# Performance work log

Hardware: AMD Instinct MI355X
Metric: run time of the kernel (lower is better)

## Reference

```python
import jax, jax.numpy as jnp
import numpy as np

B, A, S, D, OUT = 8, 16384, 2048, 512, 512
REDUCTION = "mean"  # matches init_kwargs


def setup_inputs() -> dict:
    key = jax.random.key(0)
    k1, k2, k3 = jax.random.split(key, 3)
    input_rep = jax.random.normal(k1, (B, A, D), jnp.float32)
    # sorted residue ids per protein (atoms are stored residue-by-residue)
    aa_res_ids = jnp.sort(jax.random.randint(k2, (B, A), 0, S), axis=-1).astype(jnp.int32)
    input_aa_len = jnp.full((B,), A, jnp.int32)
    input_seq_len = jnp.full((B,), S, jnp.int32)
    W = jax.random.normal(k3, (OUT, D), jnp.float32) / np.sqrt(D)
    bias = jnp.zeros((OUT,), jnp.float32)
    return {"input_rep": input_rep, "aa_res_ids": aa_res_ids,
            "input_aa_len": input_aa_len, "input_seq_len": input_seq_len,
            "W": W, "bias": bias}


def _pool(input_rep, aa_res_ids, input_aa_len, input_seq_len):
    # input_rep: [B, A, D]; aa_res_ids: [B, A] in [0, S)
    Bv, Av, Dv = input_rep.shape
    valid = jnp.arange(Av)[None, :] < input_aa_len[:, None]          # [B, A] atoms within aa_len
    seg = jnp.arange(Bv)[:, None] * S + aa_res_ids                   # flatten (b, res_id) -> segment id
    seg = jnp.where(valid, seg, Bv * S)                              # invalid atoms -> dummy segment
    nseg = Bv * S + 1
    seg_f = seg.reshape(-1)
    counts = jax.ops.segment_sum(valid.reshape(-1).astype(input_rep.dtype), seg_f,
                                 num_segments=nseg)[: Bv * S].reshape(Bv, S)
    if REDUCTION == "mean":
        sums = jax.ops.segment_sum(input_rep.reshape(Bv * Av, Dv), seg_f,
                                   num_segments=nseg)[: Bv * S].reshape(Bv, S, Dv)
        pooled = sums / jnp.maximum(counts, 1)[..., None]
    elif REDUCTION == "max":
        vals = jnp.where(valid[..., None], input_rep, -jnp.inf).reshape(Bv * Av, Dv)
        pooled = jax.ops.segment_max(vals, seg_f, num_segments=nseg)[: Bv * S].reshape(Bv, S, Dv)
        pooled = jnp.where((counts > 0)[..., None], pooled, 0.0)
    else:
        raise ValueError("Unsupported reduction method: {}".format(REDUCTION))
    in_seq = jnp.arange(S)[None, :] < input_seq_len[:, None]         # [B, S] positions within seq_len
    filled = (counts > 0) & in_seq                                   # residues that received >=1 atom
    n_fill = filled.sum(axis=1)                                      # [B]
    avg = (pooled * filled[..., None]).sum(axis=1) / jnp.maximum(n_fill, 1)[:, None].astype(input_rep.dtype)
    # unfilled-but-in-range positions get the per-protein average of filled residues; out-of-range stay 0
    out = jnp.where(filled[..., None], pooled,
                    jnp.where(in_seq[..., None], avg[:, None, :], jnp.zeros((), input_rep.dtype)))
    return out


def reference(input_rep, aa_res_ids, input_aa_len, input_seq_len, W, bias):
    out = _pool(input_rep, aa_res_ids, input_aa_len, input_seq_len)  # [B, S, D]
    return out @ W.T + bias                                          # [B, S, OUT]
```

## Files before the change

### kernel.cpp

```cpp
#include <hip/hip_runtime.h>
#include <cstdint>
#include <cstddef>

#define Bv 8
#define Av 16384
#define Sv 2048
#define Dv 512
#define OUTv 512
#define Mv (Bv * Sv)

using u16 = unsigned short;
using f32x4 = __attribute__((ext_vector_type(4))) float;
using bf16x8 = __attribute__((ext_vector_type(8))) short;

__device__ __forceinline__ u16 f2bf(float x) {
  union { float f; uint32_t u; } v; v.f = x;
  uint32_t u = v.u;
  uint32_t r = u + 0x7FFFu + ((u >> 16) & 1u);
  return (u16)(r >> 16);
}
__device__ __forceinline__ float bf2f(u16 h) {
  union { uint32_t u; float f; } v; v.u = ((uint32_t)h) << 16; return v.f;
}

__global__ __launch_bounds__(128)
void pool_kernel(const float* __restrict__ rep, const int* __restrict__ res_ids,
                 const int* __restrict__ aa_len, u16* __restrict__ pooled,
                 int* __restrict__ counts) {
  const int bs = blockIdx.x;
  const int b = bs >> 11;
  const int s = bs & (Sv - 1);
  int alen = aa_len[b];
  alen = alen < 0 ? 0 : (alen > Av ? Av : alen);
  const int* ids = res_ids + b * Av;
  int lo = 0, hi = alen;
  while (lo < hi) { int mid = (lo + hi) >> 1; if (ids[mid] < s) lo = mid + 1; else hi = mid; }
  const int start = lo;
  hi = alen;
  while (lo < hi) { int mid = (lo + hi) >> 1; if (ids[mid] <= s) lo = mid + 1; else hi = mid; }
  const int end = lo;
  const int cnt = end - start;

  const int t = threadIdx.x;
  float a0 = 0.f, a1 = 0.f, a2 = 0.f, a3 = 0.f;
  const float* base = rep + (size_t)b * Av * Dv + t * 4;
  for (int a = start; a < end; ++a) {
    float4 v = *(const float4*)(base + (size_t)a * Dv);
    a0 += v.x; a1 += v.y; a2 += v.z; a3 += v.w;
  }
  const float inv = cnt > 0 ? 1.0f / (float)cnt : 0.0f;
  ushort4 o = { f2bf(a0 * inv), f2bf(a1 * inv), f2bf(a2 * inv), f2bf(a3 * inv) };
  *(ushort4*)(pooled + (size_t)bs * Dv + t * 4) = o;
  if (t == 0) counts[bs] = cnt;
}

__global__ __launch_bounds__(256)
void wconv_kernel(const float* __restrict__ W, u16* __restrict__ Wb) {
  const int i = (blockIdx.x * 256 + threadIdx.x) * 4;
  float4 v = *(const float4*)(W + i);
  ushort4 o = { f2bf(v.x), f2bf(v.y), f2bf(v.z), f2bf(v.w) };
  *(ushort4*)(Wb + i) = o;
}

__global__ __launch_bounds__(128)
void avg_kernel(const u16* __restrict__ pooled, const int* __restrict__ counts,
                const int* __restrict__ seq_len, float* __restrict__ avg_sum,
                int* __restrict__ n_fill) {
  const int b = blockIdx.x;
  const int chunk = blockIdx.y;
  const int t = threadIdx.x;
  int slen = seq_len[b];
  slen = slen < 0 ? 0 : (slen > Sv ? Sv : slen);
  const int s0 = chunk * 128;
  float a0 = 0.f, a1 = 0.f, a2 = 0.f, a3 = 0.f;
  int filled = 0;
  for (int s = s0; s < s0 + 128; ++s) {
    if (s < slen && counts[b * Sv + s] > 0) {
      ++filled;
      ushort4 v = *(const ushort4*)(pooled + ((size_t)(b * Sv + s)) * Dv + t * 4);
      a0 += bf2f(v.x); a1 += bf2f(v.y); a2 += bf2f(v.z); a3 += bf2f(v.w);
    }
  }
  atomicAdd(&avg_sum[b * Dv + t * 4 + 0], a0);
  atomicAdd(&avg_sum[b * Dv + t * 4 + 1], a1);
  atomicAdd(&avg_sum[b * Dv + t * 4 + 2], a2);
  atomicAdd(&avg_sum[b * Dv + t * 4 + 3], a3);
  if (t == 0) atomicAdd(&n_fill[b], filled);
}

__global__ __launch_bounds__(64)
void fixup_kernel(u16* __restrict__ pooled, const int* __restrict__ counts,
                  const int* __restrict__ seq_len, const float* __restrict__ avg_sum,
                  const int* __restrict__ n_fill) {
  const int bs = blockIdx.x;
  const int b = bs >> 11;
  const int s = bs & (Sv - 1);
  int slen = seq_len[b];
  slen = slen < 0 ? 0 : (slen > Sv ? Sv : slen);
  const int cnt = counts[bs];
  const int t = threadIdx.x;
  if (s >= slen) {
    if (cnt != 0) {
      ushort4 z = {0, 0, 0, 0};
      *(ushort4*)(pooled + (size_t)bs * Dv + t * 8) = z;
      *(ushort4*)(pooled + (size_t)bs * Dv + t * 8 + 4) = z;
    }
    return;
  }
  if (cnt > 0) return;
  const int nf = n_fill[b];
  const float inv = 1.0f / (float)(nf > 0 ? nf : 1);
  float4 v0 = *(const float4*)(avg_sum + b * Dv + t * 8);
  float4 v1 = *(const float4*)(avg_sum + b * Dv + t * 8 + 4);
  ushort4 o0 = { f2bf(v0.x * inv), f2bf(v0.y * inv), f2bf(v0.z * inv), f2bf(v0.w * inv) };
  ushort4 o1 = { f2bf(v1.x * inv), f2bf(v1.y * inv), f2bf(v1.z * inv), f2bf(v1.w * inv) };
  *(ushort4*)(pooled + (size_t)bs * Dv + t * 8) = o0;
  *(ushort4*)(pooled + (size_t)bs * Dv + t * 8 + 4) = o1;
}

#define BM 128
#define BN 128
#define BK 32
#define LDT 40

__global__ __launch_bounds__(256, 2)
void gemm_kernel(const u16* __restrict__ A, const u16* __restrict__ Bw,
                 const float* __restrict__ bias, float* __restrict__ out) {
  __shared__ u16 As[BM * LDT];
  __shared__ u16 Bs[BN * LDT];
  const int tid = threadIdx.x;
  const int m0 = blockIdx.x * BM;
  const int n0 = blockIdx.y * BN;
  const int lane = tid & 63;
  const int wave = tid >> 6;
  const int wm = (wave & 1) * 64;
  const int wn = (wave >> 1) * 64;
  const int fr = lane & 15;
  const int fq = lane >> 4;

  f32x4 acc[4][4];
#pragma unroll
  for (int i = 0; i < 4; ++i)
#pragma unroll
    for (int j = 0; j < 4; ++j) acc[i][j] = (f32x4){0.f, 0.f, 0.f, 0.f};

  const int r0 = tid >> 2, kc0 = (tid & 3) * 8;
  const int r1 = (tid + 256) >> 2, kc1 = ((tid + 256) & 3) * 8;

  for (int k0 = 0; k0 < Dv; k0 += BK) {
    __syncthreads();
    *(bf16x8*)(As + r0 * LDT + kc0) = *(const bf16x8*)(A + (size_t)(m0 + r0) * Dv + k0 + kc0);
    *(bf16x8*)(As + r1 * LDT + kc1) = *(const bf16x8*)(A + (size_t)(m0 + r1) * Dv + k0 + kc1);
    *(bf16x8*)(Bs + r0 * LDT + kc0) = *(const bf16x8*)(Bw + (size_t)(n0 + r0) * Dv + k0 + kc0);
    *(bf16x8*)(Bs + r1 * LDT + kc1) = *(const bf16x8*)(Bw + (size_t)(n0 + r1) * Dv + k0 + kc1);
    __syncthreads();

    bf16x8 af[4], bfr[4];
#pragma unroll
    for (int mi = 0; mi < 4; ++mi)
      af[mi] = *(const bf16x8*)(As + (wm + mi * 16 + fr) * LDT + fq * 8);
#pragma unroll
    for (int ni = 0; ni < 4; ++ni)
      bfr[ni] = *(const bf16x8*)(Bs + (wn + ni * 16 + fr) * LDT + fq * 8);
#pragma unroll
    for (int mi = 0; mi < 4; ++mi)
#pragma unroll
      for (int ni = 0; ni < 4; ++ni)
        acc[mi][ni] = __builtin_amdgcn_mfma_f32_16x16x32_bf16(af[mi], bfr[ni], acc[mi][ni], 0, 0, 0);
  }

#pragma unroll
  for (int mi = 0; mi < 4; ++mi) {
#pragma unroll
    for (int ni = 0; ni < 4; ++ni) {
      const int col = n0 + wn + ni * 16 + fr;
      const float bv = bias[col];
#pragma unroll
      for (int r = 0; r < 4; ++r) {
        const int row = m0 + wm + mi * 16 + fq * 4 + r;
        out[(size_t)row * OUTv + col] = acc[mi][ni][r] + bv;
      }
    }
  }
}

extern "C" void kernel_launch(void* const* d_in, const int* in_sizes, int n_in,
                              void* d_out, int out_size, void* d_ws, size_t ws_size,
                              hipStream_t stream) {
  (void)in_sizes; (void)n_in; (void)out_size; (void)ws_size;
  const float* rep     = (const float*)d_in[0];
  const int*   res_ids = (const int*)d_in[1];
  const int*   aa_len  = (const int*)d_in[2];
  const int*   seq_len = (const int*)d_in[3];
  const float* W       = (const float*)d_in[4];
  const float* bias    = (const float*)d_in[5];
  float* out = (float*)d_out;

  char* ws = (char*)d_ws;
  u16*   pooled  = (u16*)ws;
  u16*   Wb      = (u16*)(ws + 16777216);
  int*   counts  = (int*)(ws + 17301504);
  float* avg_sum = (float*)(ws + 17367040);
  int*   n_fill  = (int*)(ws + 17383424);

  hipMemsetAsync(avg_sum, 0, Bv * Dv * sizeof(float) + Bv * sizeof(int), stream);

  wconv_kernel<<<(OUTv * Dv) / (256 * 4), 256, 0, stream>>>(W, Wb);
  pool_kernel<<<Mv, 128, 0, stream>>>(rep, res_ids, aa_len, pooled, counts);
  avg_kernel<<<dim3(Bv, 16), 128, 0, stream>>>(pooled, counts, seq_len, avg_sum, n_fill);
  fixup_kernel<<<Mv, 64, 0, stream>>>(pooled, counts, seq_len, avg_sum, n_fill);
  gemm_kernel<<<dim3(Mv / BM, OUTv / BN), 256, 0, stream>>>(pooled, Wb, bias, out);
}
```

Baseline: 449.5 us.

## Precompute segment start offsets and fuse weight conversion and zeroing into init kernel

Replaces the per-block binary searches over residue ids with a precomputed CSR-style starts array built by one init kernel, which also converts W to bf16 and zeroes the accumulators, removing the memset and the separate conversion launch. The pool kernel reads two offsets, unrolls its accumulation loop by two, and writes zeros directly for out-of-range rows. The avg and fixup kernels are restructured to use flags held in shared memory and one thread per row. The main cost, streaming the 268MB input, is unchanged, so the gains come only from launch and search overhead.

```diff
diff --git a/kernel.cpp b/kernel.cpp
--- a/kernel.cpp
+++ b/kernel.cpp
@@ -8,6 +8,7 @@
 #define Dv 512
 #define OUTv 512
 #define Mv (Bv * Sv)
+#define SP1 (Sv + 1)
 
 using u16 = unsigned short;
 using f32x4 = __attribute__((ext_vector_type(4))) float;
@@ -22,100 +23,137 @@
 __device__ __forceinline__ float bf2f(u16 h) {
   union { uint32_t u; float f; } v; v.u = ((uint32_t)h) << 16; return v.f;
 }
+__device__ __forceinline__ int clamp_len(int x, int hi) {
+  return x < 0 ? 0 : (x > hi ? hi : x);
+}
+
+#define NBLK_STARTS ((Bv * Av) / 256)
+#define NBLK_WCONV  ((OUTv * Dv) / (256 * 4))
+
+__global__ __launch_bounds__(256)
+void init_kernel(const int* __restrict__ res_ids, const int* __restrict__ aa_len,
+                 const float* __restrict__ W, int* __restrict__ starts,
+                 u16* __restrict__ Wb, float* __restrict__ avg_sum,
+                 int* __restrict__ n_fill) {
+  const int blk = blockIdx.x;
+  const int t = threadIdx.x;
+  if (blk < NBLK_STARTS) {
+    const int gid = blk * 256 + t;
+    if (gid < Bv * Dv) avg_sum[gid] = 0.0f;
+    if (gid < Bv) n_fill[gid] = 0;
+    const int b = gid >> 14;
+    const int a = gid & (Av - 1);
+    const int alen = clamp_len(aa_len[b], Av);
+    const int* ids = res_ids + b * Av;
+    int* st = starts + b * SP1;
+    if (alen == 0) {
+      if (a == 0) for (int s = 0; s <= Sv; ++s) st[s] = 0;
+      return;
+    }
+    if (a >= alen) return;
+    int cur = ids[a];  cur = cur < 0 ? 0 : (cur > Sv - 1 ? Sv - 1 : cur);
+    int prev = (a == 0) ? -1 : ids[a - 1];
+    prev = prev < -1 ? -1 : (prev > Sv - 1 ? Sv - 1 : prev);
+    for (int s = prev + 1; s <= cur; ++s) st[s] = a;
+    if (a == alen - 1) for (int s = cur + 1; s <= Sv; ++s) st[s] = alen;
+  } else {
+    const int i = ((blk - NBLK_STARTS) * 256 + t) * 4;
+    float4 v = *(const float4*)(W + i);
+    ushort4 o = { f2bf(v.x), f2bf(v.y), f2bf(v.z), f2bf(v.w) };
+    *(ushort4*)(Wb + i) = o;
+  }
+}
 
 __global__ __launch_bounds__(128)
-void pool_kernel(const float* __restrict__ rep, const int* __restrict__ res_ids,
-                 const int* __restrict__ aa_len, u16* __restrict__ pooled,
-                 int* __restrict__ counts) {
+void pool_kernel(const float* __restrict__ rep, const int* __restrict__ starts,
+                 const int* __restrict__ seq_len, u16* __restrict__ pooled) {
   const int bs = blockIdx.x;
   const int b = bs >> 11;
   const int s = bs & (Sv - 1);
-  int alen = aa_len[b];
-  alen = alen < 0 ? 0 : (alen > Av ? Av : alen);
-  const int* ids = res_ids + b * Av;
-  int lo = 0, hi = alen;
-  while (lo < hi) { int mid = (lo + hi) >> 1; if (ids[mid] < s) lo = mid + 1; else hi = mid; }
-  const int start = lo;
-  hi = alen;
-  while (lo < hi) { int mid = (lo + hi) >> 1; if (ids[mid] <= s) lo = mid + 1; else hi = mid; }
-  const int end = lo;
+  const int t = threadIdx.x;
+  u16* orow = pooled + (size_t)bs * Dv + t * 4;
+  const int slen = clamp_len(seq_len[b], Sv);
+  if (s >= slen) {
+    ushort4 z = {0, 0, 0, 0};
+    *(ushort4*)orow = z;
+    return;
+  }
+  const int start = starts[b * SP1 + s];
+  const int end   = starts[b * SP1 + s + 1];
   const int cnt = end - start;
 
-  const int t = threadIdx.x;
-  float a0 = 0.f, a1 = 0.f, a2 = 0.f, a3 = 0.f;
+  f32x4 acc = (f32x4){0.f, 0.f, 0.f, 0.f};
   const float* base = rep + (size_t)b * Av * Dv + t * 4;
-  for (int a = start; a < end; ++a) {
-    float4 v = *(const float4*)(base + (size_t)a * Dv);
-    a0 += v.x; a1 += v.y; a2 += v.z; a3 += v.w;
-  }
+  int a = start;
+  for (; a + 2 <= end; a += 2) {
+    f32x4 v0 = *(const f32x4*)(base + (size_t)a * Dv);
+    f32x4 v1 = *(const f32x4*)(base + (size_t)(a + 1) * Dv);
+    acc += v0; acc += v1;
+  }
+  if (a < end) acc += *(const f32x4*)(base + (size_t)a * Dv);
+
   const float inv = cnt > 0 ? 1.0f / (float)cnt : 0.0f;
-  ushort4 o = { f2bf(a0 * inv), f2bf(a1 * inv), f2bf(a2 * inv), f2bf(a3 * inv) };
-  *(ushort4*)(pooled + (size_t)bs * Dv + t * 4) = o;
-  if (t == 0) counts[bs] = cnt;
+  ushort4 o = { f2bf(acc[0] * inv), f2bf(acc[1] * inv),
+                f2bf(acc[2] * inv), f2bf(acc[3] * inv) };
+  *(ushort4*)orow = o;
 }
 
 __global__ __launch_bounds__(256)
-void wconv_kernel(const float* __restrict__ W, u16* __restrict__ Wb) {
-  const int i = (blockIdx.x * 256 + threadIdx.x) * 4;
-  float4 v = *(const float4*)(W + i);
-  ushort4 o = { f2bf(v.x), f2bf(v.y), f2bf(v.z), f2bf(v.w) };
-  *(ushort4*)(Wb + i) = o;
-}
-
-__global__ __launch_bounds__(128)
-void avg_kernel(const u16* __restrict__ pooled, const int* __restrict__ counts,
+void avg_kernel(const u16* __restrict__ pooled, const int* __restrict__ starts,
                 const int* __restrict__ seq_len, float* __restrict__ avg_sum,
                 int* __restrict__ n_fill) {
+  __shared__ int flag[128];
   const int b = blockIdx.x;
   const int chunk = blockIdx.y;
   const int t = threadIdx.x;
-  int slen = seq_len[b];
-  slen = slen < 0 ? 0 : (slen > Sv ? Sv : slen);
+  const int slen = clamp_len(seq_len[b], Sv);
   const int s0 = chunk * 128;
-  float a0 = 0.f, a1 = 0.f, a2 = 0.f, a3 = 0.f;
-  int filled = 0;
-  for (int s = s0; s < s0 + 128; ++s) {
-    if (s < slen && counts[b * Sv + s] > 0) {
-      ++filled;
-      ushort4 v = *(const ushort4*)(pooled + ((size_t)(b * Sv + s)) * Dv + t * 4);
-      a0 += bf2f(v.x); a1 += bf2f(v.y); a2 += bf2f(v.z); a3 += bf2f(v.w);
+  if (t < 128) {
+    const int s = s0 + t;
+    const int st0 = starts[b * SP1 + s];
+    const int st1 = starts[b * SP1 + s + 1];
+    flag[t] = (s < slen && st1 > st0) ? 1 : 0;
+  }
+  __syncthreads();
+  float a0 = 0.f, a1 = 0.f;
+  const u16* prow = pooled + ((size_t)(b * Sv + s0)) * Dv + t * 2;
+  for (int i = 0; i < 128; ++i) {
+    if (flag[i]) {
+      uint32_t v = *(const uint32_t*)(prow + (size_t)i * Dv);
+      a0 += bf2f((u16)(v & 0xffff));
+      a1 += bf2f((u16)(v >> 16));
     }
   }
-  atomicAdd(&avg_sum[b * Dv + t * 4 + 0], a0);
-  atomicAdd(&avg_sum[b * Dv + t * 4 + 1], a1);
-  atomicAdd(&avg_sum[b * Dv + t * 4 + 2], a2);
-  atomicAdd(&avg_sum[b * Dv + t * 4 + 3], a3);
-  if (t == 0) atomicAdd(&n_fill[b], filled);
-}
-
-__global__ __launch_bounds__(64)
-void fixup_kernel(u16* __restrict__ pooled, const int* __restrict__ counts,
+  atomicAdd(&avg_sum[b * Dv + t * 2 + 0], a0);
+  atomicAdd(&avg_sum[b * Dv + t * 2 + 1], a1);
+  if (t == 0) {
+    int c = 0;
+    for (int i = 0; i < 128; ++i) c += flag[i];
+    atomicAdd(&n_fill[b], c);
+  }
+}
+
+__global__ __launch_bounds__(256)
+void fixup_kernel(u16* __restrict__ pooled, const int* __restrict__ starts,
                   const int* __restrict__ seq_len, const float* __restrict__ avg_sum,
                   const int* __restrict__ n_fill) {
-  const int bs = blockIdx.x;
-  const int b = bs >> 11;
-  const int s = bs & (Sv - 1);
-  int slen = seq_len[b];
-  slen = slen < 0 ? 0 : (slen > Sv ? Sv : slen);
-  const int cnt = counts[bs];
-  const int t = threadIdx.x;
-  if (s >= slen) {
-    if (cnt != 0) {
-      ushort4 z = {0, 0, 0, 0};
-      *(ushort4*)(pooled + (size_t)bs * Dv + t * 8) = z;
-      *(ushort4*)(pooled + (size_t)bs * Dv + t * 8 + 4) = z;
-    }
-    return;
-  }
-  if (cnt > 0) return;
+  const int b = blockIdx.x;
+  const int s = blockIdx.y * 256 + threadIdx.x;
+  const int slen = clamp_len(seq_len[b], Sv);
+  if (s >= slen) return;
+  const int st0 = starts[b * SP1 + s];
+  const int st1 = starts[b * SP1 + s + 1];
+  if (st1 > st0) return;
   const int nf = n_fill[b];
   const float inv = 1.0f / (float)(nf > 0 ? nf : 1);
-  float4 v0 = *(const float4*)(avg_sum + b * Dv + t * 8);
-  float4 v1 = *(const float4*)(avg_sum + b * Dv + t * 8 + 4);
-  ushort4 o0 = { f2bf(v0.x * inv), f2bf(v0.y * inv), f2bf(v0.z * inv), f2bf(v0.w * inv) };
-  ushort4 o1 = { f2bf(v1.x * inv), f2bf(v1.y * inv), f2bf(v1.z * inv), f2bf(v1.w * inv) };
-  *(ushort4*)(pooled + (size_t)bs * Dv + t * 8) = o0;
-  *(ushort4*)(pooled + (size_t)bs * Dv + t * 8 + 4) = o1;
+  u16* orow = pooled + (size_t)(b * Sv + s) * Dv;
+  const float* arow = avg_sum + b * Dv;
+  for (int c = 0; c < Dv; c += 4) {
+    f32x4 v = *(const f32x4*)(arow + c);
+    ushort4 o = { f2bf(v[0] * inv), f2bf(v[1] * inv),
+                  f2bf(v[2] * inv), f2bf(v[3] * inv) };
+    *(ushort4*)(orow + c) = o;
+  }
 }
 
 #define BM 128
@@ -199,15 +237,14 @@
   char* ws = (char*)d_ws;
   u16*   pooled  = (u16*)ws;
   u16*   Wb      = (u16*)(ws + 16777216);
-  int*   counts  = (int*)(ws + 17301504);
-  float* avg_sum = (float*)(ws + 17367040);
-  int*   n_fill  = (int*)(ws + 17383424);
-
-  hipMemsetAsync(avg_sum, 0, Bv * Dv * sizeof(float) + Bv * sizeof(int), stream);
-
-  wconv_kernel<<<(OUTv * Dv) / (256 * 4), 256, 0, stream>>>(W, Wb);
-  pool_kernel<<<Mv, 128, 0, stream>>>(rep, res_ids, aa_len, pooled, counts);
-  avg_kernel<<<dim3(Bv, 16), 128, 0, stream>>>(pooled, counts, seq_len, avg_sum, n_fill);
-  fixup_kernel<<<Mv, 64, 0, stream>>>(pooled, counts, seq_len, avg_sum, n_fill);
+  int*   starts  = (int*)(ws + 17301504);
+  float* avg_sum = (float*)(ws + 17367072);
+  int*   n_fill  = (int*)(ws + 17383456);
+
+  init_kernel<<<NBLK_STARTS + NBLK_WCONV, 256, 0, stream>>>(
+      res_ids, aa_len, W, starts, Wb, avg_sum, n_fill);
+  pool_kernel<<<Mv, 128, 0, stream>>>(rep, starts, seq_len, pooled);
+  avg_kernel<<<dim3(Bv, 16), 256, 0, stream>>>(pooled, starts, seq_len, avg_sum, n_fill);
+  fixup_kernel<<<dim3(Bv, Sv / 256), 256, 0, stream>>>(pooled, starts, seq_len, avg_sum, n_fill);
   gemm_kernel<<<dim3(Mv / BM, OUTv / BN), 256, 0, stream>>>(pooled, Wb, bias, out);
 }
```

Result: no change. 451.6 us (+0.5%).
